# Optimization experiments

Measured on AMD Instinct MI355X. Metric: run time of the kernel, lower is better.

## Reference

```python
import jax, jax.numpy as jnp
import numpy as np

B, F, N = 8, 2048, 10000   # batch, features_dim, n_tiles
J, R = 10, 20
H1, H2 = 200, 100


def setup_inputs() -> dict:
    key = jax.random.key(0)
    ks = jax.random.split(key, 8)
    s = lambda fan_in: 1.0 / np.sqrt(fan_in)
    return {
        "x": jax.random.normal(ks[0], (B, F, N), dtype=jnp.float32),
        "conv_w": jax.random.uniform(ks[1], (J, F), jnp.float32, -s(F), s(F)),
        "conv_b": jax.random.uniform(ks[2], (J,), jnp.float32, -s(F), s(F)),
        "w1": jax.random.uniform(ks[3], (2 * R * J, H1), jnp.float32, -s(2 * R * J), s(2 * R * J)),
        "b1": jnp.zeros((H1,), jnp.float32),
        "w2": jax.random.uniform(ks[4], (H1, H2), jnp.float32, -s(H1), s(H1)),
        "b2": jnp.zeros((H2,), jnp.float32),
        "w3": jax.random.uniform(ks[5], (H2, 2), jnp.float32, -s(H2), s(H2)),
        "b3": jnp.zeros((2,), jnp.float32),
    }


def reference(x, conv_w, conv_b, w1, b1, w2, b2, w3, b3):
    # 1x1 Conv1d: [B,F,N] x [J,F] -> [B,J,N]
    emb = jnp.einsum("bfn,jf->bjn", x, conv_w) + conv_b[None, :, None]
    # MinMax: top-R (descending) and bottom-R (also in descending order,
    # matching the tail of a descending full sort).
    top_vals, _ = jax.lax.top_k(emb, R)                    # [B,J,R] descending
    neg_bot, _ = jax.lax.top_k(-emb, R)                    # smallest R, ascending in value
    bot_vals = jnp.flip(-neg_bot, axis=2)                  # [B,J,R] descending
    mm = jnp.concatenate([top_vals, bot_vals], axis=2)     # [B,J,2R]
    h = mm.reshape(mm.shape[0], -1)                        # [B, 2*R*J]
    h = jax.nn.sigmoid(h @ w1 + b1)
    h = jax.nn.sigmoid(h @ w2 + b2)
    return h @ w3 + b3                                     # [B, 2] logits
```

## Files before the change

### kernel.cpp

```cpp
#include <hip/hip_runtime.h>
#include <math.h>
#include <float.h>

#define B_   8
#define F_   2048
#define N_   10000
#define J_   10
#define R_   20
#define H1_  200
#define H2_  100

#define FC_     8
#define FCHUNK  (F_ / FC_)
#define VN      2
#define T1      256
#define NPB     (T1 * VN)
#define NB      ((N_ + NPB - 1) / NPB)

__global__ __launch_bounds__(T1) void conv_kernel(
    const float* __restrict__ x, const float* __restrict__ w,
    float* __restrict__ emb)
{
    const int tid = threadIdx.x;
    const int nb  = blockIdx.x;
    const int b   = blockIdx.y;
    const int fc  = blockIdx.z;

    const int n0 = nb * NPB + tid * VN;
    if (n0 >= N_) return;
    const int fbeg = fc * FCHUNK;

    const float* px = x + ((size_t)b * F_ + fbeg) * N_ + n0;
    const float* pw = w + fbeg;

    float ax[J_], ay[J_];
#pragma unroll
    for (int j = 0; j < J_; ++j) { ax[j] = 0.f; ay[j] = 0.f; }

#pragma unroll 4
    for (int f = 0; f < FCHUNK; ++f) {
        const float2 xv = *(const float2*)px;
        px += N_;
#pragma unroll
        for (int j = 0; j < J_; ++j) {
            const float wv = pw[j * F_ + f];
            ax[j] = fmaf(wv, xv.x, ax[j]);
            ay[j] = fmaf(wv, xv.y, ay[j]);
        }
    }

    float* pe = emb + (size_t)b * J_ * N_ + n0;
#pragma unroll
    for (int j = 0; j < J_; ++j) {
        atomicAdd(pe + (size_t)j * N_,     ax[j]);
        atomicAdd(pe + (size_t)j * N_ + 1, ay[j]);
    }
}

#define T2  256
#define LPT 20

__global__ __launch_bounds__(T2) void select_kernel(
    const float* __restrict__ emb, const float* __restrict__ conv_b,
    float* __restrict__ mm)
{
    __shared__ float ls_top[T2 * LPT];
    __shared__ float ls_bot[T2 * LPT];
    __shared__ float s_val[8];
    __shared__ int   s_tid[8];
    __shared__ float s_wv;
    __shared__ int   s_wt;

    const int tid = threadIdx.x;
    const int j   = blockIdx.x;
    const int b   = blockIdx.y;

    const float* row = emb + ((size_t)b * J_ + j) * N_;

    float top[LPT], bot[LPT];
#pragma unroll
    for (int k = 0; k < LPT; ++k) { top[k] = -FLT_MAX; bot[k] = FLT_MAX; }

    for (int n = tid; n < N_; n += T2) {
        const float v = row[n];
        float tv = v;
#pragma unroll
        for (int k = 0; k < LPT; ++k) {
            if (tv > top[k]) { const float o = top[k]; top[k] = tv; tv = o; }
        }
        float bv = v;
#pragma unroll
        for (int k = 0; k < LPT; ++k) {
            if (bv < bot[k]) { const float o = bot[k]; bot[k] = bv; bv = o; }
        }
    }
#pragma unroll
    for (int k = 0; k < LPT; ++k) {
        ls_top[tid * LPT + k] = top[k];
        ls_bot[tid * LPT + k] = bot[k];
    }
    __syncthreads();

    const float bias = conv_b[j];
    float* out = mm + ((size_t)b * J_ + j) * (2 * R_);

    const int lane = tid & 63;
    const int wv_  = tid >> 6;
    int ht = 0, hb = 0;

    for (int r = 0; r < R_; ++r) {
        {
            float v = ls_top[tid * LPT + ht];
            int   t = tid;
            for (int off = 32; off; off >>= 1) {
                const float vo = __shfl_down(v, off);
                const int   to = __shfl_down(t, off);
                if (vo > v) { v = vo; t = to; }
            }
            if (lane == 0) { s_val[wv_] = v; s_tid[wv_] = t; }
            __syncthreads();
            if (tid == 0) {
                float bv2 = s_val[0]; int bt = s_tid[0];
                for (int q = 1; q < T2 / 64; ++q)
                    if (s_val[q] > bv2) { bv2 = s_val[q]; bt = s_tid[q]; }
                s_wv = bv2; s_wt = bt;
            }
            __syncthreads();
            if (tid == s_wt) { ht++; out[r] = s_wv + bias; }
            __syncthreads();
        }
        {
            float v = ls_bot[tid * LPT + hb];
            int   t = tid;
            for (int off = 32; off; off >>= 1) {
                const float vo = __shfl_down(v, off);
                const int   to = __shfl_down(t, off);
                if (vo < v) { v = vo; t = to; }
            }
            if (lane == 0) { s_val[wv_] = v; s_tid[wv_] = t; }
            __syncthreads();
            if (tid == 0) {
                float bv2 = s_val[0]; int bt = s_tid[0];
                for (int q = 1; q < T2 / 64; ++q)
                    if (s_val[q] < bv2) { bv2 = s_val[q]; bt = s_tid[q]; }
                s_wv = bv2; s_wt = bt;
            }
            __syncthreads();
            if (tid == s_wt) { hb++; out[2 * R_ - 1 - r] = s_wv + bias; }
            __syncthreads();
        }
    }
}

__global__ __launch_bounds__(256) void mlp_kernel(
    const float* __restrict__ mm,
    const float* __restrict__ w1, const float* __restrict__ b1,
    const float* __restrict__ w2, const float* __restrict__ b2,
    const float* __restrict__ w3, const float* __restrict__ b3,
    float* __restrict__ out)
{
    __shared__ float h0[2 * R_ * J_];
    __shared__ float h1[H1_];
    __shared__ float h2[H2_];

    const int tid = threadIdx.x;
    const int b   = blockIdx.x;

    for (int i = tid; i < 2 * R_ * J_; i += 256) h0[i] = mm[b * 2 * R_ * J_ + i];
    __syncthreads();

    if (tid < H1_) {
        float acc = b1[tid];
#pragma unroll 4
        for (int i = 0; i < 2 * R_ * J_; ++i)
            acc = fmaf(h0[i], w1[i * H1_ + tid], acc);
        h1[tid] = 1.f / (1.f + expf(-acc));
    }
    __syncthreads();

    if (tid < H2_) {
        float acc = b2[tid];
#pragma unroll 4
        for (int i = 0; i < H1_; ++i)
            acc = fmaf(h1[i], w2[i * H2_ + tid], acc);
        h2[tid] = 1.f / (1.f + expf(-acc));
    }
    __syncthreads();

    if (tid < 2) {
        float acc = b3[tid];
        for (int i = 0; i < H2_; ++i)
            acc = fmaf(h2[i], w3[i * 2 + tid], acc);
        out[b * 2 + tid] = acc;
    }
}

extern "C" void kernel_launch(void* const* d_in, const int* in_sizes, int n_in,
                              void* d_out, int out_size, void* d_ws, size_t ws_size,
                              hipStream_t stream)
{
    const float* x      = (const float*)d_in[0];
    const float* conv_w = (const float*)d_in[1];
    const float* conv_b = (const float*)d_in[2];
    const float* w1     = (const float*)d_in[3];
    const float* b1     = (const float*)d_in[4];
    const float* w2     = (const float*)d_in[5];
    const float* b2     = (const float*)d_in[6];
    const float* w3     = (const float*)d_in[7];
    const float* b3     = (const float*)d_in[8];

    float* emb = (float*)d_ws;
    float* mm  = emb + (size_t)B_ * J_ * N_;
    float* out = (float*)d_out;

    hipMemsetAsync(emb, 0, (size_t)B_ * J_ * N_ * sizeof(float), stream);

    conv_kernel<<<dim3(NB, B_, FC_), T1, 0, stream>>>(x, conv_w, emb);
    select_kernel<<<dim3(J_, B_), T2, 0, stream>>>(emb, conv_b, mm);
    mlp_kernel<<<B_, 256, 0, stream>>>(mm, w1, b1, w2, b2, w3, b3, out);
}
```

Baseline: 963.5 us.

## Replace atomic conv reduction with per-chunk partial planes summed in select

The conv kernel now writes each F-chunk's partial sums to its own plane with float4 stores, replacing per-element atomicAdd and removing the memset. The select kernel sums the 16 partial planes while it scans each row. The change also doubles the F split to 16 and widens each thread to 4 columns, so grid shape and per-thread register use both change. In exchange it needs 16x more workspace and adds a strided 16-plane read to the low-parallelism select kernel.

```diff
diff --git a/kernel.cpp b/kernel.cpp
--- a/kernel.cpp
+++ b/kernel.cpp
@@ -10,16 +10,17 @@
 #define H1_  200
 #define H2_  100
 
-#define FC_     8
+#define FC_     16
 #define FCHUNK  (F_ / FC_)
-#define VN      2
+#define VN      4
 #define T1      256
 #define NPB     (T1 * VN)
 #define NB      ((N_ + NPB - 1) / NPB)
+#define PLANE   ((size_t)B_ * J_ * N_)
 
 __global__ __launch_bounds__(T1) void conv_kernel(
     const float* __restrict__ x, const float* __restrict__ w,
-    float* __restrict__ emb)
+    float* __restrict__ part)
 {
     const int tid = threadIdx.x;
     const int nb  = blockIdx.x;
@@ -33,27 +34,28 @@
     const float* px = x + ((size_t)b * F_ + fbeg) * N_ + n0;
     const float* pw = w + fbeg;
 
-    float ax[J_], ay[J_];
-#pragma unroll
-    for (int j = 0; j < J_; ++j) { ax[j] = 0.f; ay[j] = 0.f; }
-
-#pragma unroll 4
+    float4 acc[J_];
+#pragma unroll
+    for (int j = 0; j < J_; ++j) acc[j] = make_float4(0.f, 0.f, 0.f, 0.f);
+
+#pragma unroll 2
     for (int f = 0; f < FCHUNK; ++f) {
-        const float2 xv = *(const float2*)px;
+        const float4 xv = *(const float4*)px;
         px += N_;
 #pragma unroll
         for (int j = 0; j < J_; ++j) {
             const float wv = pw[j * F_ + f];
-            ax[j] = fmaf(wv, xv.x, ax[j]);
-            ay[j] = fmaf(wv, xv.y, ay[j]);
-        }
-    }
-
-    float* pe = emb + (size_t)b * J_ * N_ + n0;
+            acc[j].x = fmaf(wv, xv.x, acc[j].x);
+            acc[j].y = fmaf(wv, xv.y, acc[j].y);
+            acc[j].z = fmaf(wv, xv.z, acc[j].z);
+            acc[j].w = fmaf(wv, xv.w, acc[j].w);
+        }
+    }
+
+    float* pe = part + (size_t)fc * PLANE + ((size_t)b * J_) * N_ + n0;
 #pragma unroll
     for (int j = 0; j < J_; ++j) {
-        atomicAdd(pe + (size_t)j * N_,     ax[j]);
-        atomicAdd(pe + (size_t)j * N_ + 1, ay[j]);
+        *(float4*)(pe + (size_t)j * N_) = acc[j];
     }
 }
 
@@ -61,7 +63,7 @@
 #define LPT 20
 
 __global__ __launch_bounds__(T2) void select_kernel(
-    const float* __restrict__ emb, const float* __restrict__ conv_b,
+    const float* __restrict__ part, const float* __restrict__ conv_b,
     float* __restrict__ mm)
 {
     __shared__ float ls_top[T2 * LPT];
@@ -75,14 +77,17 @@
     const int j   = blockIdx.x;
     const int b   = blockIdx.y;
 
-    const float* row = emb + ((size_t)b * J_ + j) * N_;
+    const float* row = part + ((size_t)b * J_ + j) * N_;
 
     float top[LPT], bot[LPT];
 #pragma unroll
     for (int k = 0; k < LPT; ++k) { top[k] = -FLT_MAX; bot[k] = FLT_MAX; }
 
     for (int n = tid; n < N_; n += T2) {
-        const float v = row[n];
+        float v = 0.f;
+#pragma unroll
+        for (int fc = 0; fc < FC_; ++fc) v += row[(size_t)fc * PLANE + n];
+
         float tv = v;
 #pragma unroll
         for (int k = 0; k < LPT; ++k) {
@@ -209,13 +214,11 @@
     const float* w3     = (const float*)d_in[7];
     const float* b3     = (const float*)d_in[8];
 
-    float* emb = (float*)d_ws;
-    float* mm  = emb + (size_t)B_ * J_ * N_;
-    float* out = (float*)d_out;
-
-    hipMemsetAsync(emb, 0, (size_t)B_ * J_ * N_ * sizeof(float), stream);
-
-    conv_kernel<<<dim3(NB, B_, FC_), T1, 0, stream>>>(x, conv_w, emb);
-    select_kernel<<<dim3(J_, B_), T2, 0, stream>>>(emb, conv_b, mm);
+    float* part = (float*)d_ws;
+    float* mm   = part + (size_t)FC_ * PLANE;
+    float* out  = (float*)d_out;
+
+    conv_kernel<<<dim3(NB, B_, FC_), T1, 0, stream>>>(x, conv_w, part);
+    select_kernel<<<dim3(J_, B_), T2, 0, stream>>>(part, conv_b, mm);
     mlp_kernel<<<B_, 256, 0, stream>>>(mm, w1, b1, w2, b2, w3, b3, out);
 }
```

Result: no change. 956.9 us (-0.7%).
